# Performance work log

Hardware: AMD Instinct MI355X
Metric: run time of the kernel (lower is better)

The kernel has to match this reference:

```python
import jax, jax.numpy as jnp
import numpy as np

EPS = 1e-5

def conv1d(x, w, b, pad):
    # x: [B,C_in,S], w: [C_out,C_in,K] -> [B,C_out,S]
    y = jax.lax.conv_general_dilated(x, w, window_strides=(1,), padding=[(pad, pad)],
                                     dimension_numbers=('NCH', 'OIH', 'NCH'))
    return y + b[None, :, None]

def bn(x, gamma, beta, mean, var):
    # inference-mode BatchNorm1d over channel dim of [B,C,S]
    scale = gamma * jax.lax.rsqrt(var + EPS)
    shift = beta - mean * scale
    return x * scale[None, :, None] + shift[None, :, None]

def setup_inputs() -> dict:
    key = jax.random.key(0)
    ks = jax.random.split(key, 16)
    B, S, D, C, K = 32, 2048, 128, 256, 5
    x = jax.random.normal(ks[0], (B, S, D), dtype=jnp.float32)
    start_padding_indices = jax.random.randint(ks[1], (B,), 0, S, dtype=jnp.int64 if jax.config.jax_enable_x64 else jnp.int32)
    def conv_init(k, co, ci, kk):
        fan = ci * kk
        return jax.random.normal(k, (co, ci, kk), dtype=jnp.float32) / np.sqrt(fan)
    W1 = conv_init(ks[2], C, D, K); b1 = jnp.zeros((C,), jnp.float32)
    g1 = jnp.ones((C,), jnp.float32); be1 = jnp.zeros((C,), jnp.float32)
    m1 = jax.random.normal(ks[3], (C,), dtype=jnp.float32) * 0.1
    v1 = jax.random.uniform(ks[4], (C,), dtype=jnp.float32, minval=0.5, maxval=1.5)
    W2 = conv_init(ks[5], C, C, K); b2 = jnp.zeros((C,), jnp.float32)
    g2 = jnp.ones((C,), jnp.float32); be2 = jnp.zeros((C,), jnp.float32)
    m2 = jax.random.normal(ks[6], (C,), dtype=jnp.float32) * 0.1
    v2 = jax.random.uniform(ks[7], (C,), dtype=jnp.float32, minval=0.5, maxval=1.5)
    Wf = conv_init(ks[8], D, C, 1); bf = jnp.zeros((D,), jnp.float32)
    return {"x": x, "start_padding_indices": start_padding_indices,
            "W1": W1, "b1": b1, "g1": g1, "be1": be1, "m1": m1, "v1": v1,
            "W2": W2, "b2": b2, "g2": g2, "be2": be2, "m2": m2, "v2": v2,
            "Wf": Wf, "bf": bf}

def reference(x, start_padding_indices, W1, b1, g1, be1, m1, v1,
              W2, b2, g2, be2, m2, v2, Wf, bf):
    B, S, D = x.shape
    K = W1.shape[-1]
    h = jnp.transpose(x, (0, 2, 1))                      # [B,D,S]
    h = jax.nn.relu(bn(conv1d(h, W1, b1, K // 2), g1, be1, m1, v1))
    h = jax.nn.relu(bn(conv1d(h, W2, b2, K // 2), g2, be2, m2, v2))
    h = conv1d(h, Wf, bf, 0)                             # [B,D,S]
    conv_out = jnp.transpose(h, (0, 2, 1))               # [B,S,D]
    # vectorized masked mean: -1 sentinel -> full length; 0 -> zeros
    lengths = jnp.where(start_padding_indices == -1, S, start_padding_indices)  # [B]
    mask = jnp.arange(S)[None, :] < lengths[:, None]     # [B,S]
    sums = jnp.sum(conv_out * mask[:, :, None].astype(conv_out.dtype), axis=1)  # [B,D]
    denom = jnp.maximum(lengths, 1).astype(conv_out.dtype)[:, None]
    pooled = jnp.where(lengths[:, None] > 0, sums / denom, jnp.zeros_like(sums))
    return pooled
```

## Files before the change

### kernel.cpp

```cpp
#include <hip/hip_runtime.h>

#define S_LEN 2048
#define NBATCH 32

typedef __bf16 bf16x8 __attribute__((ext_vector_type(8)));
typedef float f32x4 __attribute__((ext_vector_type(4)));
typedef unsigned short bf_t;

__device__ __forceinline__ unsigned short f2bf(float f) {
  __bf16 h = (__bf16)f;
  return __builtin_bit_cast(unsigned short, h);
}

#if __has_builtin(__builtin_amdgcn_global_load_lds)
#define USE_GLL 1
#else
#define USE_GLL 0
#endif

__device__ __forceinline__ void load_lds16(const void* g, void* ldsbase) {
#if USE_GLL
  __builtin_amdgcn_global_load_lds(
      (const __attribute__((address_space(1))) unsigned int*)g,
      (__attribute__((address_space(3))) unsigned int*)ldsbase, 16, 0, 0);
#else
  *(int4*)((char*)ldsbase + (threadIdx.x & 63) * 16) =
      *(const int4*)((const char*)g);
#endif
}

#define WAITV8  asm volatile("s_waitcnt vmcnt(8)" ::: "memory")
#define WAITV4  asm volatile("s_waitcnt vmcnt(4)" ::: "memory")
#define WAITV0  asm volatile("s_waitcnt vmcnt(0)" ::: "memory")

__global__ void prep_all(const float* __restrict__ x,
                         const float* __restrict__ W1, const float* __restrict__ W2,
                         const float* __restrict__ b1, const float* __restrict__ g1,
                         const float* __restrict__ be1, const float* __restrict__ m1,
                         const float* __restrict__ v1,
                         const float* __restrict__ b2, const float* __restrict__ g2,
                         const float* __restrict__ be2, const float* __restrict__ m2,
                         const float* __restrict__ v2,
                         bf_t* __restrict__ xb, bf_t* __restrict__ wf1,
                         bf_t* __restrict__ wf2,
                         float* __restrict__ abuf, float* __restrict__ zp) {
  const int bid = blockIdx.x;
  if (bid < 4096) {
    const size_t i = (size_t)bid * 256 + threadIdx.x;
    const float4 a = ((const float4*)x)[2 * i];
    const float4 c = ((const float4*)x)[2 * i + 1];
    ushort4 o0; o0.x = f2bf(a.x); o0.y = f2bf(a.y); o0.z = f2bf(a.z); o0.w = f2bf(a.w);
    ushort4 o1; o1.x = f2bf(c.x); o1.y = f2bf(c.y); o1.z = f2bf(c.z); o1.w = f2bf(c.w);
    ((ushort4*)xb)[2 * i] = o0;
    ((ushort4*)xb)[2 * i + 1] = o1;
  } else if (bid < 6016) {
    const float* w; bf_t* wfm; int idx; int CIN;
    if (bid < 4736) { w = W1; wfm = wf1; idx = (bid - 4096) * 256 + threadIdx.x; CIN = 128; }
    else            { w = W2; wfm = wf2; idx = (bid - 4736) * 256 + threadIdx.x; CIN = 256; }
    const int TAPS = 5;
    const int j = idx & 7;
    const int l = (idx >> 3) & 63;
    const int f = (idx >> 9) & 7;
    const int wr = (idx >> 12) & 1;
    const int tg = idx >> 13;
    const int co = wr * 128 + f * 16 + (l & 15);
    const int cc = tg / (TAPS * 4);
    const int k = (tg / 4) % TAPS;
    const int q = tg & 3;
    const int ci = cc * 128 + q * 32 + (l >> 4) * 8 + j;
    wfm[idx] = f2bf(w[((size_t)co * CIN + ci) * TAPS + k]);
  } else {
    int c = threadIdx.x;
    if (c < 64) zp[c] = 0.f;
    if (c < 256) {
      float a1 = g1[c] * rsqrtf(v1[c] + 1e-5f);
      abuf[c] = a1;
      abuf[256 + c] = (b1[c] - m1[c]) * a1 + be1[c];
      float a2 = g2[c] * rsqrtf(v2[c] + 1e-5f);
      abuf[512 + c] = a2;
      abuf[768 + c] = (b2[c] - m2[c]) * a2 + be2[c];
    }
  }
}

template <int CIN, int TAPS, bool POOL>
__device__ __forceinline__ void conv_body(
    const bf_t* __restrict__ xin, const bf_t* __restrict__ wfm,
    const float* __restrict__ alpha, const float* __restrict__ bias,
    const float* __restrict__ zp, bf_t* __restrict__ hout,
    const int* __restrict__ spi, float* __restrict__ hpart) {
  constexpr int HALO = (TAPS - 1) / 2;
  constexpr int P = (CIN / 128) * TAPS * 4;
  constexpr int NKT = P / 2;

  __shared__ char smem[131072];

  const int tid = threadIdx.x;
  const int l = tid & 63;
  const int wv = tid >> 6;
  const int wr = wv >> 2;
  const int wn = wv & 3;
  const int b = blockIdx.x >> 3;
  const int s0 = (blockIdx.x & 7) << 8;
  const int l15 = l & 15;
  const int l4 = l >> 4;
  const int wu16 = (tid - l) * 16;

  f32x4 acc[8][4] = {};

  auto STAGE_A = [&](int jt, int sub) {
    const char* src = (const char*)wfm + (size_t)(2 * jt + sub) * 16384;
    char* dst = smem + (jt & 1) * 32768 + sub * 16384;
    load_lds16(src + tid * 16, dst + wu16);
    load_lds16(src + 8192 + tid * 16, dst + 8192 + wu16);
  };

  auto STAGE_B = [&](int jt, int sub) {
    const int t = 2 * jt + sub;
    const int cc = t / (TAPS * 4);
    const int k = (t >> 2) % TAPS;
    const int q = t & 3;
    char* dst = smem + 65536 + (jt & 1) * 32768 + sub * 16384;
    const int r0 = tid >> 2;
    const int slot = ((r0 & 3) ^ ((r0 >> 2) & 3)) << 4;
    const char* srcb = (const char*)xin +
        ((size_t)b * S_LEN * CIN + cc * 128 + q * 32) * 2 +
        (((tid & 3) * 16) ^ slot);
    {
      const int s = s0 + r0 - HALO + k;
      const char* src = ((unsigned)s < (unsigned)S_LEN)
          ? srcb + (size_t)s * (CIN * 2) : ((const char*)zp + (((tid & 3) * 16) ^ slot));
      load_lds16(src, dst + wu16);
    }
    {
      const int s = s0 + r0 + 128 - HALO + k;
      const char* src = ((unsigned)s < (unsigned)S_LEN)
          ? srcb + (size_t)s * (CIN * 2) : ((const char*)zp + (((tid & 3) * 16) ^ slot));
      load_lds16(src, dst + 8192 + wu16);
    }
  };

  auto LDB = [&](const char* Bb, int sub, int r) -> bf16x8 {
    const int slot = (((r & 3) ^ ((r >> 2) & 3)) << 4);
    return *(const bf16x8*)(Bb + sub * 16384 + r * 64 + ((l4 * 16) ^ slot));
  };

  STAGE_A(0, 0); STAGE_A(0, 1); STAGE_B(0, 0); STAGE_B(0, 1);
  WAITV0;
  STAGE_A(1, 0); STAGE_B(1, 0);
  __builtin_amdgcn_s_barrier();

#pragma unroll 1
  for (int j = 0; j < NKT; ++j) {
    const char* Ab = smem + (j & 1) * 32768;
    const char* Bb = smem + 65536 + (j & 1) * 32768;

    {
      __builtin_amdgcn_s_setprio(1);
      bf16x8 afr[8], bfr[4];
#pragma unroll
      for (int f = 0; f < 8; ++f)
        afr[f] = *(const bf16x8*)(Ab + wr * 8192 + f * 1024 + l * 16);
#pragma unroll
      for (int n = 0; n < 4; ++n)
        bfr[n] = LDB(Bb, 0, wn * 64 + n * 16 + l15);
      if (j + 1 < NKT) { STAGE_B(j + 1, 1); STAGE_A(j + 1, 1); }
#pragma unroll
      for (int f = 0; f < 8; ++f)
#pragma unroll
        for (int n = 0; n < 4; ++n)
          acc[f][n] = __builtin_amdgcn_mfma_f32_16x16x32_bf16(
              afr[f], bfr[n], acc[f][n], 0, 0, 0);
      __builtin_amdgcn_s_setprio(0);
      if (j < NKT - 1) { WAITV8; } else { WAITV0; }
      __builtin_amdgcn_s_barrier();
      __builtin_amdgcn_sched_barrier(0);
    }

    {
      __builtin_amdgcn_s_setprio(1);
      bf16x8 afr[8], bfr[4];
#pragma unroll
      for (int f = 0; f < 8; ++f)
        afr[f] = *(const bf16x8*)(Ab + 16384 + wr * 8192 + f * 1024 + l * 16);
#pragma unroll
      for (int n = 0; n < 4; ++n)
        bfr[n] = LDB(Bb, 1, wn * 64 + n * 16 + l15);
      if (j + 2 < NKT) { STAGE_A(j + 2, 0); STAGE_B(j + 2, 0); }
#pragma unroll
      for (int f = 0; f < 8; ++f)
#pragma unroll
        for (int n = 0; n < 4; ++n)
          acc[f][n] = __builtin_amdgcn_mfma_f32_16x16x32_bf16(
              afr[f], bfr[n], acc[f][n], 0, 0, 0);
      __builtin_amdgcn_s_setprio(0);
      if (j <= NKT - 3) { WAITV8; } else if (j == NKT - 2) { WAITV4; }
      __builtin_amdgcn_s_barrier();
      __builtin_amdgcn_sched_barrier(0);
    }
  }

  WAITV0;
  __syncthreads();

  if constexpr (!POOL) {
    const int cobase = wr * 128;
#pragma unroll
    for (int f = 0; f < 8; ++f) {
      const int co0 = cobase + f * 16 + l4 * 4;
      const f32x4 al = *(const f32x4*)(alpha + co0);
      const f32x4 bi = *(const f32x4*)(bias + co0);
#pragma unroll
      for (int n = 0; n < 4; ++n) {
        const int sp = wn * 64 + n * 16 + l15;
        ushort4 pk;
        pk.x = f2bf(fmaxf(acc[f][n][0] * al[0] + bi[0], 0.f));
        pk.y = f2bf(fmaxf(acc[f][n][1] * al[1] + bi[1], 0.f));
        pk.z = f2bf(fmaxf(acc[f][n][2] * al[2] + bi[2], 0.f));
        pk.w = f2bf(fmaxf(acc[f][n][3] * al[3] + bi[3], 0.f));
        *(ushort4*)(smem + sp * 512 + ((co0 * 2) ^ ((sp & 7) << 4))) = pk;
      }
    }
    __syncthreads();
    char* hb = (char*)hout + ((size_t)(b * S_LEN + s0) * 256) * 2;
#pragma unroll
    for (int k = 0; k < 16; ++k) {
      const int c = tid + k * 512;
      const int sp = c >> 5;
      const int col = (c & 31) * 16;
      const int4 v = *(const int4*)(smem + sp * 512 + (col ^ ((sp & 7) << 4)));
      *(int4*)(hb + (size_t)sp * 512 + col) = v;
    }
  } else {
    float* red = (float*)smem;
    int len = spi[b];
    if (len < 0) len = S_LEN;
    const int cobase = wr * 128;
#pragma unroll
    for (int f = 0; f < 8; ++f) {
      const int co0 = cobase + f * 16 + l4 * 4;
      const f32x4 al = *(const f32x4*)(alpha + co0);
      const f32x4 bi = *(const f32x4*)(bias + co0);
      f32x4 vs = {};
#pragma unroll
      for (int n = 0; n < 4; ++n) {
        const int s = s0 + wn * 64 + n * 16 + l15;
        const float m = (s < len) ? 1.f : 0.f;
        vs[0] += fmaxf(acc[f][n][0] * al[0] + bi[0], 0.f) * m;
        vs[1] += fmaxf(acc[f][n][1] * al[1] + bi[1], 0.f) * m;
        vs[2] += fmaxf(acc[f][n][2] * al[2] + bi[2], 0.f) * m;
        vs[3] += fmaxf(acc[f][n][3] * al[3] + bi[3], 0.f) * m;
      }
#pragma unroll
      for (int d = 1; d < 16; d <<= 1) {
        vs[0] += __shfl_xor(vs[0], d, 64);
        vs[1] += __shfl_xor(vs[1], d, 64);
        vs[2] += __shfl_xor(vs[2], d, 64);
        vs[3] += __shfl_xor(vs[3], d, 64);
      }
      if (l15 == 0) {
        float* rp = red + ((wv * 8 + f) * 4 + l4) * 4;
        rp[0] = vs[0]; rp[1] = vs[1]; rp[2] = vs[2]; rp[3] = vs[3];
      }
    }
    __syncthreads();
    if (tid < 256) {
      const int co = tid;
      const int wrc = co >> 7;
      const int fc = (co >> 4) & 7;
      const int l4c = (co >> 2) & 3;
      const int jc = co & 3;
      float s = 0.f;
#pragma unroll
      for (int w = 0; w < 4; ++w)
        s += red[(((wrc * 4 + w) * 8 + fc) * 4 + l4c) * 4 + jc];
      const int pt = blockIdx.x & 7;
      hpart[((size_t)b * 8 + pt) * 256 + co] = s;
    }
  }
}

__global__ __launch_bounds__(512, 2)
void conv_gemm_L1(const bf_t* __restrict__ xin, const bf_t* __restrict__ wfm,
                  const float* __restrict__ alpha, const float* __restrict__ bias,
                  const float* __restrict__ zp, bf_t* __restrict__ hout) {
  conv_body<128, 5, false>(xin, wfm, alpha, bias, zp, hout, nullptr, nullptr);
}

__global__ __launch_bounds__(512, 2)
void conv_gemm_L2(const bf_t* __restrict__ xin, const bf_t* __restrict__ wfm,
                  const float* __restrict__ alpha, const float* __restrict__ bias,
                  const float* __restrict__ zp, const int* __restrict__ spi,
                  float* __restrict__ hpart) {
  conv_body<256, 5, true>(xin, wfm, alpha, bias, zp, nullptr, spi, hpart);
}

__global__ void pool_matvec(const float* __restrict__ hpart,
                            const float* __restrict__ Wf,
                            const float* __restrict__ bf_,
                            const int* __restrict__ spi,
                            float* __restrict__ out) {
  __shared__ float S[256];
  const int b = blockIdx.x;
  const int tid = threadIdx.x;
  for (int c = tid; c < 256; c += 128) {
    float s = 0.f;
#pragma unroll
    for (int pt = 0; pt < 8; ++pt) s += hpart[((size_t)b * 8 + pt) * 256 + c];
    S[c] = s;
  }
  __syncthreads();
  int len = spi[b];
  if (len < 0) len = S_LEN;
  float a = 0.f;
  const float* wrow = Wf + (size_t)tid * 256;
  for (int c = 0; c < 256; ++c) a += wrow[c] * S[c];
  float res = 0.f;
  if (len > 0) res = (a + (float)len * bf_[tid]) / (float)len;
  out[b * 128 + tid] = res;
}

extern "C" void kernel_launch(void* const* d_in, const int* in_sizes, int n_in,
                              void* d_out, int out_size, void* d_ws, size_t ws_size,
                              hipStream_t stream) {
  (void)in_sizes; (void)n_in; (void)out_size; (void)ws_size;
  const float* x = (const float*)d_in[0];
  const int* spi = (const int*)d_in[1];
  const float* W1 = (const float*)d_in[2];
  const float* b1 = (const float*)d_in[3];
  const float* g1 = (const float*)d_in[4];
  const float* be1 = (const float*)d_in[5];
  const float* m1 = (const float*)d_in[6];
  const float* v1 = (const float*)d_in[7];
  const float* W2 = (const float*)d_in[8];
  const float* b2 = (const float*)d_in[9];
  const float* g2 = (const float*)d_in[10];
  const float* be2 = (const float*)d_in[11];
  const float* m2 = (const float*)d_in[12];
  const float* v2 = (const float*)d_in[13];
  const float* Wf = (const float*)d_in[14];
  const float* bf_ = (const float*)d_in[15];
  float* out = (float*)d_out;

  char* ws = (char*)d_ws;
  float* zp   = (float*)(ws);
  bf_t* xb    = (bf_t*)(ws + 4096);
  bf_t* h1    = (bf_t*)(ws + 16781312);
  bf_t* wf1   = (bf_t*)(ws + 83890176);
  bf_t* wf2   = (bf_t*)(ws + 84217856);
  float* abuf = (float*)(ws + 84938752);
  float* hpart= (float*)(ws + 84942848);

  prep_all<<<6017, 256, 0, stream>>>(x, W1, W2,
                                     b1, g1, be1, m1, v1,
                                     b2, g2, be2, m2, v2,
                                     xb, wf1, wf2, abuf, zp);
  conv_gemm_L1<<<256, 512, 0, stream>>>(xb, wf1, abuf, abuf + 256, zp, h1);
  conv_gemm_L2<<<256, 512, 0, stream>>>(h1, wf2, abuf + 512, abuf + 768, zp,
                                        spi, hpart);
  pool_matvec<<<32, 128, 0, stream>>>(hpart, Wf, bf_, spi, out);
}
```

Baseline: 88.25 us.

## Fuse fp32-to-bf16 input conversion into first conv GEMM B-tile staging

Removes the separate x conversion pass from the prep kernel and has the layer-1 conv load fp32 x directly, converting to bf16 in registers and writing to LDS. This drops a 16MB read plus 8MB write round trip through the workspace. In exchange, layer 1 loses async global-to-LDS loads for the B tile, adds register conversion work, reads each x row five times (once per tap) in fp32, and uses tighter waitcnt/lgkm waits that may reduce load/compute overlap.

New measurement: 92.33 us. +4.6%, slower.

```diff
diff --git a/kernel.cpp b/kernel.cpp
--- a/kernel.cpp
+++ b/kernel.cpp
@@ -31,32 +31,24 @@
 
 #define WAITV8  asm volatile("s_waitcnt vmcnt(8)" ::: "memory")
 #define WAITV4  asm volatile("s_waitcnt vmcnt(4)" ::: "memory")
+#define WAITV2  asm volatile("s_waitcnt vmcnt(2)" ::: "memory")
 #define WAITV0  asm volatile("s_waitcnt vmcnt(0)" ::: "memory")
-
-__global__ void prep_all(const float* __restrict__ x,
-                         const float* __restrict__ W1, const float* __restrict__ W2,
+#define LGKM0   asm volatile("s_waitcnt lgkmcnt(0)" ::: "memory")
+
+__global__ void prep_all(const float* __restrict__ W1, const float* __restrict__ W2,
                          const float* __restrict__ b1, const float* __restrict__ g1,
                          const float* __restrict__ be1, const float* __restrict__ m1,
                          const float* __restrict__ v1,
                          const float* __restrict__ b2, const float* __restrict__ g2,
                          const float* __restrict__ be2, const float* __restrict__ m2,
                          const float* __restrict__ v2,
-                         bf_t* __restrict__ xb, bf_t* __restrict__ wf1,
-                         bf_t* __restrict__ wf2,
+                         bf_t* __restrict__ wf1, bf_t* __restrict__ wf2,
                          float* __restrict__ abuf, float* __restrict__ zp) {
   const int bid = blockIdx.x;
-  if (bid < 4096) {
-    const size_t i = (size_t)bid * 256 + threadIdx.x;
-    const float4 a = ((const float4*)x)[2 * i];
-    const float4 c = ((const float4*)x)[2 * i + 1];
-    ushort4 o0; o0.x = f2bf(a.x); o0.y = f2bf(a.y); o0.z = f2bf(a.z); o0.w = f2bf(a.w);
-    ushort4 o1; o1.x = f2bf(c.x); o1.y = f2bf(c.y); o1.z = f2bf(c.z); o1.w = f2bf(c.w);
-    ((ushort4*)xb)[2 * i] = o0;
-    ((ushort4*)xb)[2 * i + 1] = o1;
-  } else if (bid < 6016) {
+  if (bid < 1920) {
     const float* w; bf_t* wfm; int idx; int CIN;
-    if (bid < 4736) { w = W1; wfm = wf1; idx = (bid - 4096) * 256 + threadIdx.x; CIN = 128; }
-    else            { w = W2; wfm = wf2; idx = (bid - 4736) * 256 + threadIdx.x; CIN = 256; }
+    if (bid < 640) { w = W1; wfm = wf1; idx = bid * 256 + threadIdx.x; CIN = 128; }
+    else           { w = W2; wfm = wf2; idx = (bid - 640) * 256 + threadIdx.x; CIN = 256; }
     const int TAPS = 5;
     const int j = idx & 7;
     const int l = (idx >> 3) & 63;
@@ -83,9 +75,9 @@
   }
 }
 
-template <int CIN, int TAPS, bool POOL>
+template <int CIN, int TAPS, bool POOL, bool F32IN>
 __device__ __forceinline__ void conv_body(
-    const bf_t* __restrict__ xin, const bf_t* __restrict__ wfm,
+    const void* __restrict__ xin, const bf_t* __restrict__ wfm,
     const float* __restrict__ alpha, const float* __restrict__ bias,
     const float* __restrict__ zp, bf_t* __restrict__ hout,
     const int* __restrict__ spi, float* __restrict__ hpart) {
@@ -117,26 +109,40 @@
 
   auto STAGE_B = [&](int jt, int sub) {
     const int t = 2 * jt + sub;
-    const int cc = t / (TAPS * 4);
     const int k = (t >> 2) % TAPS;
     const int q = t & 3;
     char* dst = smem + 65536 + (jt & 1) * 32768 + sub * 16384;
     const int r0 = tid >> 2;
     const int slot = ((r0 & 3) ^ ((r0 >> 2) & 3)) << 4;
-    const char* srcb = (const char*)xin +
-        ((size_t)b * S_LEN * CIN + cc * 128 + q * 32) * 2 +
-        (((tid & 3) * 16) ^ slot);
-    {
-      const int s = s0 + r0 - HALO + k;
-      const char* src = ((unsigned)s < (unsigned)S_LEN)
-          ? srcb + (size_t)s * (CIN * 2) : ((const char*)zp + (((tid & 3) * 16) ^ slot));
-      load_lds16(src, dst + wu16);
-    }
-    {
-      const int s = s0 + r0 + 128 - HALO + k;
-      const char* src = ((unsigned)s < (unsigned)S_LEN)
-          ? srcb + (size_t)s * (CIN * 2) : ((const char*)zp + (((tid & 3) * 16) ^ slot));
-      load_lds16(src, dst + 8192 + wu16);
+    const int col = ((tid & 3) * 16) ^ slot;
+    if constexpr (F32IN) {
+      const char* xrow = (const char*)xin + ((size_t)b * S_LEN * 128) * 4 +
+                         q * 128 + col * 2;
+#pragma unroll
+      for (int h = 0; h < 2; ++h) {
+        const int s = s0 + (tid >> 2) + h * 128 - HALO + k;
+        const char* src = ((unsigned)s < (unsigned)S_LEN)
+            ? xrow + (size_t)s * 512 : ((const char*)zp + col * 2);
+        const float4 a = *(const float4*)(src);
+        const float4 c = *(const float4*)(src + 16);
+        int4 v;
+        v.x = (int)((unsigned)f2bf(a.x) | ((unsigned)f2bf(a.y) << 16));
+        v.y = (int)((unsigned)f2bf(a.z) | ((unsigned)f2bf(a.w) << 16));
+        v.z = (int)((unsigned)f2bf(c.x) | ((unsigned)f2bf(c.y) << 16));
+        v.w = (int)((unsigned)f2bf(c.z) | ((unsigned)f2bf(c.w) << 16));
+        *(int4*)(dst + h * 8192 + tid * 16) = v;
+      }
+    } else {
+      const int cc = t / (TAPS * 4);
+      const char* srcb = (const char*)xin +
+          ((size_t)b * S_LEN * CIN + cc * 128 + q * 32) * 2 + col;
+#pragma unroll
+      for (int h = 0; h < 2; ++h) {
+        const int s = s0 + r0 + h * 128 - HALO + k;
+        const char* src = ((unsigned)s < (unsigned)S_LEN)
+            ? srcb + (size_t)s * (CIN * 2) : ((const char*)zp + col);
+        load_lds16(src, dst + h * 8192 + wu16);
+      }
     }
   };
 
@@ -147,7 +153,9 @@
 
   STAGE_A(0, 0); STAGE_A(0, 1); STAGE_B(0, 0); STAGE_B(0, 1);
   WAITV0;
+  if constexpr (F32IN) LGKM0;
   STAGE_A(1, 0); STAGE_B(1, 0);
+  if constexpr (F32IN) LGKM0;
   __builtin_amdgcn_s_barrier();
 
 #pragma unroll 1
@@ -172,7 +180,12 @@
           acc[f][n] = __builtin_amdgcn_mfma_f32_16x16x32_bf16(
               afr[f], bfr[n], acc[f][n], 0, 0, 0);
       __builtin_amdgcn_s_setprio(0);
-      if (j < NKT - 1) { WAITV8; } else { WAITV0; }
+      if constexpr (F32IN) {
+        if (j < NKT - 1) { WAITV2; } else { WAITV0; }
+        LGKM0;
+      } else {
+        if (j < NKT - 1) { WAITV8; } else { WAITV0; }
+      }
       __builtin_amdgcn_s_barrier();
       __builtin_amdgcn_sched_barrier(0);
     }
@@ -194,7 +207,12 @@
           acc[f][n] = __builtin_amdgcn_mfma_f32_16x16x32_bf16(
               afr[f], bfr[n], acc[f][n], 0, 0, 0);
       __builtin_amdgcn_s_setprio(0);
-      if (j <= NKT - 3) { WAITV8; } else if (j == NKT - 2) { WAITV4; }
+      if constexpr (F32IN) {
+        if (j < NKT - 1) { WAITV2; } else { WAITV0; }
+        LGKM0;
+      } else {
+        if (j <= NKT - 3) { WAITV8; } else if (j == NKT - 2) { WAITV4; }
+      }
       __builtin_amdgcn_s_barrier();
       __builtin_amdgcn_sched_barrier(0);
     }
@@ -281,10 +299,10 @@
 }
 
 __global__ __launch_bounds__(512, 2)
-void conv_gemm_L1(const bf_t* __restrict__ xin, const bf_t* __restrict__ wfm,
+void conv_gemm_L1(const float* __restrict__ xin, const bf_t* __restrict__ wfm,
                   const float* __restrict__ alpha, const float* __restrict__ bias,
                   const float* __restrict__ zp, bf_t* __restrict__ hout) {
-  conv_body<128, 5, false>(xin, wfm, alpha, bias, zp, hout, nullptr, nullptr);
+  conv_body<128, 5, false, true>(xin, wfm, alpha, bias, zp, hout, nullptr, nullptr);
 }
 
 __global__ __launch_bounds__(512, 2)
@@ -292,7 +310,7 @@
                   const float* __restrict__ alpha, const float* __restrict__ bias,
                   const float* __restrict__ zp, const int* __restrict__ spi,
                   float* __restrict__ hpart) {
-  conv_body<256, 5, true>(xin, wfm, alpha, bias, zp, nullptr, spi, hpart);
+  conv_body<256, 5, true, false>(xin, wfm, alpha, bias, zp, nullptr, spi, hpart);
 }
 
 __global__ void pool_matvec(const float* __restrict__ hpart,
@@ -344,18 +362,17 @@
 
   char* ws = (char*)d_ws;
   float* zp   = (float*)(ws);
-  bf_t* xb    = (bf_t*)(ws + 4096);
   bf_t* h1    = (bf_t*)(ws + 16781312);
   bf_t* wf1   = (bf_t*)(ws + 83890176);
   bf_t* wf2   = (bf_t*)(ws + 84217856);
   float* abuf = (float*)(ws + 84938752);
   float* hpart= (float*)(ws + 84942848);
 
-  prep_all<<<6017, 256, 0, stream>>>(x, W1, W2,
+  prep_all<<<1921, 256, 0, stream>>>(W1, W2,
                                      b1, g1, be1, m1, v1,
                                      b2, g2, be2, m2, v2,
-                                     xb, wf1, wf2, abuf, zp);
-  conv_gemm_L1<<<256, 512, 0, stream>>>(xb, wf1, abuf, abuf + 256, zp, h1);
+                                     wf1, wf2, abuf, zp);
+  conv_gemm_L1<<<256, 512, 0, stream>>>(x, wf1, abuf, abuf + 256, zp, h1);
   conv_gemm_L2<<<256, 512, 0, stream>>>(h1, wf2, abuf + 512, abuf + 768, zp,
                                         spi, hpart);
   pool_matvec<<<32, 128, 0, stream>>>(hpart, Wf, bf_, spi, out);
```
